# Kernel tuning notes

Hardware: AMD Instinct MI355X
Metric: run time of the kernel (lower is better)

The kernel has to match this reference:

```python
import jax, jax.numpy as jnp
import numpy as np

BIGINT = 1e10
BOA, BOH, BOL = 21, 22, 23      # global-node residue symbols
ATOM_POS_PAD = 0                # atom position pad index
AG_SEG = 1                      # antigen segment id


def setup_inputs() -> dict:
    key = jax.random.key(0)
    ks = jax.random.split(key, 8)
    B, L, C, E = 16, 128, 14, 256
    N = B * L
    # residues with global tokens at fixed positions per protein
    S = jax.random.randint(ks[0], (B, L), 0, 21)
    S = S.at[:, 0].set(BOA).at[:, 48].set(BOH).at[:, 96].set(BOL)
    S = S.reshape(N)
    seg = np.zeros((L,), np.int32); seg[0:48] = 1; seg[48:96] = 2; seg[96:] = 3
    segment_ids = jnp.tile(jnp.asarray(seg), B)
    RP = jnp.tile(jnp.arange(L, dtype=jnp.int32), B)
    A = jax.random.randint(ks[1], (N, C), 1, 16)
    AP = jax.random.randint(ks[2], (N, C), 0, 16)
    AP = AP.at[:, :4].set(jnp.arange(1, 5, dtype=AP.dtype)[None, :])  # backbone always present
    X = jax.random.normal(ks[3], (N, C, 3), dtype=jnp.float32) * 3.0
    res_embed = jax.random.normal(ks[4], (25, E), dtype=jnp.float32) * 0.02
    atom_embed = jax.random.normal(ks[5], (16, E), dtype=jnp.float32) * 0.02
    atom_pos_embed = jax.random.normal(ks[6], (16, E), dtype=jnp.float32) * 0.02
    return dict(S=S, RP=RP, A=A, AP=AP, X=X, segment_ids=segment_ids,
                res_embed=res_embed, atom_embed=atom_embed,
                atom_pos_embed=atom_pos_embed, max_n=L, k_neighbors=9)


def _embed(S, RP, A, AP, res_embed, atom_embed, atom_pos_embed):
    N = S.shape[0]
    E = res_embed.shape[1]
    half = E // 2
    inv = jnp.power(10000.0, -2.0 * jnp.arange(half, dtype=jnp.float32) / E)
    ang = RP.astype(jnp.float32)[:, None] * inv[None, :]
    pos_e = jnp.stack([jnp.sin(ang), jnp.cos(ang)], axis=-1).reshape(N, E)
    res_e = res_embed[S] + pos_e
    atom_e = atom_embed[A] + atom_pos_embed[AP]            # [N,C,E]
    not_pad = (AP != ATOM_POS_PAD)
    denom = not_pad.sum(-1, keepdims=True).astype(res_e.dtype) + 1e-10
    atom_e = jnp.sum(atom_e * not_pad[..., None], axis=1) / denom
    return jnp.concatenate([res_e, atom_e], axis=-1)       # [N,2E]


def _min_pair_dist(X, AP, max_n):
    # min over atom pairs of ||X[i,a]-X[j,b]||, pad atoms pushed to BIGINT
    N, C, _ = X.shape
    B = N // max_n
    Xb = X.reshape(B, max_n, C, 3)
    pad = (AP == ATOM_POS_PAD).reshape(B, max_n, C)
    sq = jnp.sum(Xb * Xb, axis=-1)                          # [B,L,C]
    dot = jnp.einsum('biad,bjcd->biajc', Xb, Xb)            # [B,L,C,L,C]
    d2 = sq[:, :, :, None, None] + sq[:, None, None, :, :] - 2.0 * dot
    dist = jnp.sqrt(jnp.maximum(d2, 0.0))
    pmask = pad[:, :, :, None, None] | pad[:, None, None, :, :]
    dist = dist + pmask.astype(dist.dtype) * BIGINT
    return jnp.min(dist, axis=(2, 4))                       # [B,L,L]


def _knn(dist_mat, sel_mask, k):
    # smallest-k neighbors among selected candidate edges; invalid -> -1
    B, L, _ = dist_mat.shape
    d = jnp.where(sel_mask, dist_mat, BIGINT)
    neg, dst_local = jax.lax.top_k(-d, k)                   # [B,L,k]
    valid = ((-neg) < BIGINT).reshape(-1)
    offs = (jnp.arange(B) * L)[:, None, None]
    src = jnp.broadcast_to(jnp.arange(L)[None, :, None] + offs, (B, L, k)).reshape(-1)
    dst = (dst_local + offs).reshape(-1)
    src = jnp.where(valid, src, -1)
    dst = jnp.where(valid, dst, -1)
    return jnp.stack([src, dst]), valid


def reference(S, RP, A, AP, X, segment_ids, res_embed, atom_embed, atom_pos_embed, max_n, k_neighbors):
    N = S.shape[0]
    L = max_n
    B = N // L
    h = _embed(S, RP, A, AP, res_embed, atom_embed, atom_pos_embed)
    dist = _min_pair_dist(X, AP, L)                          # [B,L,L]
    g = ((S == BOA) | (S == BOH) | (S == BOL)).reshape(B, L)
    seg = segment_ids.reshape(B, L)
    not_self = ~jnp.eye(L, dtype=bool)[None]                 # exclude i==j
    gi, gj = g[:, :, None], g[:, None, :]
    not_global = ~(gi | gj)
    same_seg = seg[:, :, None] == seg[:, None, :]
    inner_mask = same_seg & not_global & not_self
    outer_mask = (~same_seg) & not_global & not_self
    ctx_knn, ctx_valid = _knn(dist, inner_mask, k_neighbors)
    inter_knn, inter_valid = _knn(dist, outer_mask, k_neighbors)
    # non-kNN ctx edges (global_normal | global_global | sequential), dense adjacency
    global_normal = same_seg & (gi | gj) & not_self
    global_global = gi & gj & not_self
    idx = jnp.arange(L)
    adj_seq = (jnp.abs(idx[:, None] - idx[None, :]) == 1)[None]
    seq_mask = adj_seq & not_global & (seg[:, :, None] != AG_SEG)
    extra_ctx_adj = global_normal | global_global | seq_mask  # [B,L,L] bool
    return h, ctx_knn, ctx_valid, extra_ctx_adj, inter_knn, inter_valid
```

## Files before the change

### kernel.cpp

```cpp
#include <hip/hip_runtime.h>
#include <math.h>
#include <float.h>
#include <stdint.h>

#define BIGINT_F 1e10f
#define L_TOK 128
#define C_ATOM 14
#define E_DIM 256
#define K_NB 9

__device__ __forceinline__ float sq3(float x, float y, float z) {
    return __fadd_rn(__fadd_rn(__fmul_rn(x, x), __fmul_rn(y, y)), __fmul_rn(z, z));
}

__device__ __forceinline__ uint64_t umin64(uint64_t a, uint64_t b) { return a < b ? a : b; }

__global__ void __launch_bounds__(256)
fused_kernel(const int* __restrict__ S, const int* __restrict__ RP,
             const int* __restrict__ A, const int* __restrict__ AP,
             const float* __restrict__ X, const int* __restrict__ seg,
             const float* __restrict__ res_embed,
             const float* __restrict__ atom_embed,
             const float* __restrict__ atom_pos_embed,
             float* __restrict__ h,
             float* __restrict__ ctx_src, float* __restrict__ ctx_dst, float* __restrict__ ctx_val,
             float* __restrict__ adj_out,
             float* __restrict__ int_src, float* __restrict__ int_dst, float* __restrict__ int_val,
             int N) {
    const int NKNN = N / 4;
    int blk = blockIdx.x;
    int tid = threadIdx.x;

    if (blk < NKNN) {
        int wave = tid >> 6;
        int lane = tid & 63;
        int bi = blk * 4 + wave;
        int b  = bi >> 7;
        int i  = bi & (L_TOK - 1);

        __shared__ float4 sxi[4][C_ATOM];
        if (lane < C_ATOM) {
            const float* xp = X + ((size_t)bi * C_ATOM + lane) * 3;
            float x0 = xp[0], x1 = xp[1], x2 = xp[2];
            float sq = (AP[bi * C_ATOM + lane] == 0) ? INFINITY : sq3(x0, x1, x2);
            sxi[wave][lane] = make_float4(x0, x1, x2, sq);
        }
        __syncthreads();

        float xa0[C_ATOM], xa1[C_ATOM], xa2[C_ATOM], sa[C_ATOM];
        #pragma unroll
        for (int a = 0; a < C_ATOM; ++a) {
            float4 t = sxi[wave][a];
            xa0[a] = t.x; xa1[a] = t.y; xa2[a] = t.z; sa[a] = t.w;
        }

        int j0 = lane, j1 = lane + 64;
        int nj0 = (b << 7) + j0, nj1 = (b << 7) + j1;

        float mind0 = INFINITY, mind1 = INFINITY;
        for (int c = 0; c < C_ATOM; ++c) {
            const float* yp0 = X + ((size_t)nj0 * C_ATOM + c) * 3;
            const float* yp1 = X + ((size_t)nj1 * C_ATOM + c) * 3;
            float y00 = yp0[0], y01 = yp0[1], y02 = yp0[2];
            float y10 = yp1[0], y11 = yp1[1], y12 = yp1[2];
            float sc0 = (AP[nj0 * C_ATOM + c] == 0) ? INFINITY : sq3(y00, y01, y02);
            float sc1 = (AP[nj1 * C_ATOM + c] == 0) ? INFINITY : sq3(y10, y11, y12);
            #pragma unroll
            for (int a = 0; a < C_ATOM; ++a) {
                float dot0 = __fadd_rn(__fadd_rn(__fmul_rn(xa0[a], y00),
                                                 __fmul_rn(xa1[a], y01)),
                                       __fmul_rn(xa2[a], y02));
                float d20 = __fsub_rn(__fadd_rn(sa[a], sc0), __fmul_rn(2.0f, dot0));
                mind0 = fminf(mind0, d20);
                float dot1 = __fadd_rn(__fadd_rn(__fmul_rn(xa0[a], y10),
                                                 __fmul_rn(xa1[a], y11)),
                                       __fmul_rn(xa2[a], y12));
                float d21 = __fsub_rn(__fadd_rn(sa[a], sc1), __fmul_rn(2.0f, dot1));
                mind1 = fminf(mind1, d21);
            }
        }
        float d0 = sqrtf(fmaxf(mind0, 0.0f));
        float d1 = sqrtf(fmaxf(mind1, 0.0f));

        int si = S[bi];
        int segi = seg[bi];
        bool gi = si >= 21;
        int sj0 = S[nj0], sj1 = S[nj1];
        int segj0 = seg[nj0], segj1 = seg[nj1];
        bool gj0 = sj0 >= 21, gj1 = sj1 >= 21;
        bool ng0 = !gi && !gj0 && (j0 != i);
        bool ng1 = !gi && !gj1 && (j1 != i);
        bool inner0 = (segi == segj0) && ng0;
        bool inner1 = (segi == segj1) && ng1;
        bool outer0 = (segi != segj0) && ng0;
        bool outer1 = (segi != segj1) && ng1;

        const uint32_t bigbits = __float_as_uint(BIGINT_F);
        uint64_t kd0 = ((uint64_t)__float_as_uint(d0) << 32) | (uint32_t)j0;
        uint64_t kd1 = ((uint64_t)__float_as_uint(d1) << 32) | (uint32_t)j1;
        uint64_t kbig0 = ((uint64_t)bigbits << 32) | (uint32_t)j0;
        uint64_t kbig1 = ((uint64_t)bigbits << 32) | (uint32_t)j1;

        for (int pass = 0; pass < 2; ++pass) {
            uint64_t k0 = (pass == 0 ? inner0 : outer0) ? kd0 : kbig0;
            uint64_t k1 = (pass == 0 ? inner1 : outer1) ? kd1 : kbig1;
            float* osrc = (pass == 0) ? ctx_src : int_src;
            float* odst = (pass == 0) ? ctx_dst : int_dst;
            float* oval = (pass == 0) ? ctx_val : int_val;
            #pragma unroll
            for (int k = 0; k < K_NB; ++k) {
                uint64_t kk = umin64(k0, k1);
                #pragma unroll
                for (int m = 32; m > 0; m >>= 1) {
                    uint64_t o = __shfl_xor((unsigned long long)kk, m, 64);
                    kk = umin64(kk, o);
                }
                if (k0 == kk) k0 = UINT64_MAX;
                if (k1 == kk) k1 = UINT64_MAX;
                if (lane == 0) {
                    uint32_t dbits = (uint32_t)(kk >> 32);
                    int jmin = (int)(uint32_t)kk;
                    bool valid = dbits < bigbits;
                    int o = bi * K_NB + k;
                    osrc[o] = valid ? (float)bi : -1.0f;
                    odst[o] = valid ? (float)((b << 7) + jmin) : -1.0f;
                    oval[o] = valid ? 1.0f : 0.0f;
                }
            }
        }
    } else if (blk < NKNN + N) {
        int n = blk - NKNN;
        int e = tid;
        int s = S[n];
        float rp = (float)RP[n];

        int k = e >> 1;
        const float c1 = (float)(-2.0 * 13.287712379549449 / (double)E_DIM);
        float invk = exp2f((float)k * c1);
        float ang = rp * invk;
        float pe = (e & 1) ? cosf(ang) : sinf(ang);
        h[(size_t)n * (2 * E_DIM) + e] = res_embed[s * E_DIM + e] + pe;

        __shared__ int sA[C_ATOM], sAP[C_ATOM];
        if (e < C_ATOM) { sA[e] = A[n * C_ATOM + e]; sAP[e] = AP[n * C_ATOM + e]; }
        __syncthreads();

        float sum = 0.0f, cnt = 0.0f;
        for (int c = 0; c < C_ATOM; ++c) {
            if (sAP[c] != 0) {
                sum += atom_embed[sA[c] * E_DIM + e] + atom_pos_embed[sAP[c] * E_DIM + e];
                cnt += 1.0f;
            }
        }
        h[(size_t)n * (2 * E_DIM) + E_DIM + e] = sum / (cnt + 1e-10f);
    } else {
        int idx = (blk - NKNN - N) * 256 + tid;
        int b = idx >> 14;
        int i = (idx >> 7) & (L_TOK - 1);
        int j = idx & (L_TOK - 1);
        int ni = (b << 7) + i, nj = (b << 7) + j;
        bool gi = S[ni] >= 21, gj = S[nj] >= 21;
        int segi = seg[ni], segj = seg[nj];
        bool notself = (i != j);
        bool same = (segi == segj);
        bool gn = same && (gi || gj) && notself;
        bool gg = gi && gj && notself;
        int d = i - j;
        bool adjacent = (d == 1 || d == -1);
        bool sm = adjacent && !(gi || gj) && (segi != 1);
        adj_out[idx] = (gn || gg || sm) ? 1.0f : 0.0f;
    }
}

extern "C" void kernel_launch(void* const* d_in, const int* in_sizes, int n_in,
                              void* d_out, int out_size, void* d_ws, size_t ws_size,
                              hipStream_t stream) {
    const int*   S    = (const int*)d_in[0];
    const int*   RP   = (const int*)d_in[1];
    const int*   A    = (const int*)d_in[2];
    const int*   AP   = (const int*)d_in[3];
    const float* X    = (const float*)d_in[4];
    const int*   seg  = (const int*)d_in[5];
    const float* rese = (const float*)d_in[6];
    const float* atme = (const float*)d_in[7];
    const float* atpe = (const float*)d_in[8];

    const int N = in_sizes[0];
    const int B = N / L_TOK;
    float* out = (float*)d_out;

    size_t off = 0;
    float* h_out   = out + off;  off += (size_t)N * 2 * E_DIM;
    float* ctx_src = out + off;  off += (size_t)N * K_NB;
    float* ctx_dst = out + off;  off += (size_t)N * K_NB;
    float* ctx_val = out + off;  off += (size_t)N * K_NB;
    float* adj_out = out + off;  off += (size_t)B * L_TOK * L_TOK;
    float* int_src = out + off;  off += (size_t)N * K_NB;
    float* int_dst = out + off;  off += (size_t)N * K_NB;
    float* int_val = out + off;  off += (size_t)N * K_NB;

    int nknn = N / 4;
    int nadj = (B * L_TOK * L_TOK) / 256;
    int grid = nknn + N + nadj;
    fused_kernel<<<grid, 256, 0, stream>>>(S, RP, A, AP, X, seg, rese, atme, atpe,
                                           h_out, ctx_src, ctx_dst, ctx_val,
                                           adj_out, int_src, int_dst, int_val, N);
}
```

Baseline: 97.45 us.

## Stage protein atom coordinates in swizzled LDS and fold adjacency into kNN blocks

```diff
diff --git a/kernel.cpp b/kernel.cpp
--- a/kernel.cpp
+++ b/kernel.cpp
@@ -37,34 +37,42 @@
         int bi = blk * 4 + wave;
         int b  = bi >> 7;
         int i  = bi & (L_TOK - 1);
-
-        __shared__ float4 sxi[4][C_ATOM];
-        if (lane < C_ATOM) {
-            const float* xp = X + ((size_t)bi * C_ATOM + lane) * 3;
-            float x0 = xp[0], x1 = xp[1], x2 = xp[2];
-            float sq = (AP[bi * C_ATOM + lane] == 0) ? INFINITY : sq3(x0, x1, x2);
-            sxi[wave][lane] = make_float4(x0, x1, x2, sq);
+        int base_tok = (b << 7);
+
+        __shared__ float sX[C_ATOM * L_TOK];
+        __shared__ float sY[C_ATOM * L_TOK];
+        __shared__ float sZ[C_ATOM * L_TOK];
+        __shared__ float sQ[C_ATOM * L_TOK];
+
+        const float* Xb  = X  + (size_t)base_tok * C_ATOM * 3;
+        const int*   APb = AP + base_tok * C_ATOM;
+        for (int idx = tid; idx < L_TOK * C_ATOM; idx += 256) {
+            int tok = idx / C_ATOM;
+            int c   = idx - tok * C_ATOM;
+            float x0 = Xb[idx * 3 + 0];
+            float x1 = Xb[idx * 3 + 1];
+            float x2 = Xb[idx * 3 + 2];
+            float q  = (APb[idx] == 0) ? INFINITY : sq3(x0, x1, x2);
+            int w = c * L_TOK + (tok ^ (2 * c));
+            sX[w] = x0; sY[w] = x1; sZ[w] = x2; sQ[w] = q;
         }
         __syncthreads();
 
         float xa0[C_ATOM], xa1[C_ATOM], xa2[C_ATOM], sa[C_ATOM];
         #pragma unroll
         for (int a = 0; a < C_ATOM; ++a) {
-            float4 t = sxi[wave][a];
-            xa0[a] = t.x; xa1[a] = t.y; xa2[a] = t.z; sa[a] = t.w;
+            int w = a * L_TOK + (i ^ (2 * a));
+            xa0[a] = sX[w]; xa1[a] = sY[w]; xa2[a] = sZ[w]; sa[a] = sQ[w];
         }
 
         int j0 = lane, j1 = lane + 64;
-        int nj0 = (b << 7) + j0, nj1 = (b << 7) + j1;
+        int nj0 = base_tok + j0, nj1 = base_tok + j1;
 
         float mind0 = INFINITY, mind1 = INFINITY;
         for (int c = 0; c < C_ATOM; ++c) {
-            const float* yp0 = X + ((size_t)nj0 * C_ATOM + c) * 3;
-            const float* yp1 = X + ((size_t)nj1 * C_ATOM + c) * 3;
-            float y00 = yp0[0], y01 = yp0[1], y02 = yp0[2];
-            float y10 = yp1[0], y11 = yp1[1], y12 = yp1[2];
-            float sc0 = (AP[nj0 * C_ATOM + c] == 0) ? INFINITY : sq3(y00, y01, y02);
-            float sc1 = (AP[nj1 * C_ATOM + c] == 0) ? INFINITY : sq3(y10, y11, y12);
+            int w = c * L_TOK + (lane ^ (2 * c));
+            float y00 = sX[w],      y01 = sY[w],      y02 = sZ[w],      sc0 = sQ[w];
+            float y10 = sX[w + 64], y11 = sY[w + 64], y12 = sZ[w + 64], sc1 = sQ[w + 64];
             #pragma unroll
             for (int a = 0; a < C_ATOM; ++a) {
                 float dot0 = __fadd_rn(__fadd_rn(__fmul_rn(xa0[a], y00),
@@ -88,12 +96,24 @@
         int sj0 = S[nj0], sj1 = S[nj1];
         int segj0 = seg[nj0], segj1 = seg[nj1];
         bool gj0 = sj0 >= 21, gj1 = sj1 >= 21;
-        bool ng0 = !gi && !gj0 && (j0 != i);
-        bool ng1 = !gi && !gj1 && (j1 != i);
+        bool ns0 = (j0 != i), ns1 = (j1 != i);
+        bool ng0 = !gi && !gj0 && ns0;
+        bool ng1 = !gi && !gj1 && ns1;
         bool inner0 = (segi == segj0) && ng0;
         bool inner1 = (segi == segj1) && ng1;
         bool outer0 = (segi != segj0) && ng0;
         bool outer1 = (segi != segj1) && ng1;
+
+        {
+            bool gij0 = gi || gj0, gij1 = gi || gj1;
+            bool same0 = (segi == segj0), same1 = (segi == segj1);
+            int dd0 = i - j0, dd1 = i - j1;
+            bool a0 = (dd0 == 1 || dd0 == -1), a1 = (dd1 == 1 || dd1 == -1);
+            bool v0 = (same0 && gij0 && ns0) || (gi && gj0 && ns0) || (a0 && !gij0 && (segi != 1));
+            bool v1 = (same1 && gij1 && ns1) || (gi && gj1 && ns1) || (a1 && !gij1 && (segi != 1));
+            adj_out[(size_t)bi * L_TOK + j0] = v0 ? 1.0f : 0.0f;
+            adj_out[(size_t)bi * L_TOK + j1] = v1 ? 1.0f : 0.0f;
+        }
 
         const uint32_t bigbits = __float_as_uint(BIGINT_F);
         uint64_t kd0 = ((uint64_t)__float_as_uint(d0) << 32) | (uint32_t)j0;
@@ -123,12 +143,12 @@
                     bool valid = dbits < bigbits;
                     int o = bi * K_NB + k;
                     osrc[o] = valid ? (float)bi : -1.0f;
-                    odst[o] = valid ? (float)((b << 7) + jmin) : -1.0f;
+                    odst[o] = valid ? (float)(base_tok + jmin) : -1.0f;
                     oval[o] = valid ? 1.0f : 0.0f;
                 }
             }
         }
-    } else if (blk < NKNN + N) {
+    } else {
         int n = blk - NKNN;
         int e = tid;
         int s = S[n];
@@ -153,22 +173,6 @@
             }
         }
         h[(size_t)n * (2 * E_DIM) + E_DIM + e] = sum / (cnt + 1e-10f);
-    } else {
-        int idx = (blk - NKNN - N) * 256 + tid;
-        int b = idx >> 14;
-        int i = (idx >> 7) & (L_TOK - 1);
-        int j = idx & (L_TOK - 1);
-        int ni = (b << 7) + i, nj = (b << 7) + j;
-        bool gi = S[ni] >= 21, gj = S[nj] >= 21;
-        int segi = seg[ni], segj = seg[nj];
-        bool notself = (i != j);
-        bool same = (segi == segj);
-        bool gn = same && (gi || gj) && notself;
-        bool gg = gi && gj && notself;
-        int d = i - j;
-        bool adjacent = (d == 1 || d == -1);
-        bool sm = adjacent && !(gi || gj) && (segi != 1);
-        adj_out[idx] = (gn || gg || sm) ? 1.0f : 0.0f;
     }
 }
 
@@ -200,8 +204,7 @@
     float* int_val = out + off;  off += (size_t)N * K_NB;
 
     int nknn = N / 4;
-    int nadj = (B * L_TOK * L_TOK) / 256;
-    int grid = nknn + N + nadj;
+    int grid = nknn + N;
     fused_kernel<<<grid, 256, 0, stream>>>(S, RP, A, AP, X, seg, rese, atme, atpe,
                                            h_out, ctx_src, ctx_dst, ctx_val,
                                            adj_out, int_src, int_dst, int_val, N);
```

After: 97.91 us. No clear change (+0.5%).
